# Kernel tuning notes

Measured on AMD Instinct MI355X. Metric: run time of the kernel, lower is better.

## Reference

```python
import jax, jax.numpy as jnp
import numpy as np

D_MODEL = 1024
NUM_HEADS = 16
HEAD_DIM = D_MODEL // NUM_HEADS
WINDOW = 64
GLOBAL_TOKENS = 4
MAX_SEQ_LEN = 2048
RANDOM_TOKENS = 32
BATCH = 2
SEQ = 2048
NEG = -1.0e9
LN_EPS = 1e-5


def setup_inputs() -> dict:
    key = jax.random.key(0)
    k1, k2, k3, k4 = jax.random.split(key, 4)
    x = jax.random.normal(k1, (BATCH, SEQ, D_MODEL), dtype=jnp.float32)
    w_qkv = jax.random.normal(k2, (D_MODEL, 3 * D_MODEL), dtype=jnp.float32) * (D_MODEL ** -0.5)
    w_out = jax.random.normal(k3, (D_MODEL, D_MODEL), dtype=jnp.float32) * (D_MODEL ** -0.5)
    ln_gamma = jnp.ones((D_MODEL,), dtype=jnp.float32)
    ln_beta = jnp.zeros((D_MODEL,), dtype=jnp.float32)
    rand_idx = jax.random.randint(k4, (MAX_SEQ_LEN, RANDOM_TOKENS), 0, MAX_SEQ_LEN, dtype=jnp.int32)
    return {"x": x, "w_qkv": w_qkv, "w_out": w_out,
            "ln_gamma": ln_gamma, "ln_beta": ln_beta, "rand_idx": rand_idx}


def _build_masks(seq_len, rand_idx):
    i = jnp.arange(seq_len)
    causal = (i[:, None] >= i[None, :]).astype(jnp.float32)  # [L,L], lower-triangular
    # local window mask
    dist = jnp.abs(i[:, None] - i[None, :])
    local = (dist <= WINDOW).astype(jnp.float32) * causal
    # global column mask: columns {0..G-1} u {L-G..L-1}, rows i >= g (== causal on those cols)
    gcols = jnp.concatenate([jnp.arange(GLOBAL_TOKENS), jnp.arange(seq_len - GLOBAL_TOKENS, seq_len)])
    is_gcol = jnp.zeros((seq_len,), jnp.float32).at[gcols].set(1.0)
    glob = is_gcol[None, :] * causal
    # random mask: per-row fixed random columns, then causal-filtered
    ri = rand_idx[:seq_len]  # [L, R]
    rows = jnp.broadcast_to(i[:, None], ri.shape)
    rnd = jnp.zeros((seq_len, seq_len), jnp.float32).at[rows, ri].set(1.0) * causal
    return local, glob, rnd


def reference(x, w_qkv, w_out, ln_gamma, ln_beta, rand_idx):
    B, L, _ = x.shape
    residual = x
    # LayerNorm
    mu = jnp.mean(x, axis=-1, keepdims=True)
    var = jnp.mean(jnp.square(x - mu), axis=-1, keepdims=True)
    xn = (x - mu) * jax.lax.rsqrt(var + LN_EPS) * ln_gamma + ln_beta
    # QKV projection
    qkv = xn @ w_qkv
    q, k, v = jnp.split(qkv, 3, axis=-1)
    q = q.reshape(B, L, NUM_HEADS, HEAD_DIM).transpose(0, 2, 1, 3)  # [B,H,L,D]
    k = k.reshape(B, L, NUM_HEADS, HEAD_DIM).transpose(0, 2, 1, 3)
    v = v.reshape(B, L, NUM_HEADS, HEAD_DIM).transpose(0, 2, 1, 3)
    local, glob, rnd = _build_masks(L, rand_idx)
    raw = jnp.einsum('bhqd,bhkd->bhqk', q, k) / jnp.sqrt(jnp.float32(HEAD_DIM))
    # original sums three masked copies of the same scores:
    # combined = 3*raw + ((1-local)+(1-glob)+(1-rnd)) * NEG
    penalty = (3.0 - (local + glob + rnd)) * NEG  # [L,L]
    combined = 3.0 * raw + penalty[None, None, :, :]
    attn = jax.nn.softmax(combined, axis=-1)
    out = jnp.einsum('bhqk,bhkd->bhqd', attn, v)
    out = out.transpose(0, 2, 1, 3).reshape(B, L, D_MODEL)
    out = out @ w_out
    return out + residual
```

## Files before the change

### kernel.cpp

```cpp
#include <hip/hip_runtime.h>
#include <stdint.h>

typedef __attribute__((ext_vector_type(8))) short shortx8;
typedef __attribute__((ext_vector_type(4))) float floatx4;

static constexpr int SEQ_    = 2048;
static constexpr int DMODEL  = 1024;
static constexpr int HDIM    = 64;
static constexpr int BATCH_  = 2;
static constexpr int NHEADS  = 16;
static constexpr int WINDOW_ = 64;
static constexpr int GTOK    = 4;
static constexpr int RTOK    = 32;
static constexpr int ROWS    = BATCH_ * SEQ_;
static constexpr int QKVN    = 3 * DMODEL;

__device__ inline unsigned short f2bf(float f) {
  union { float f; unsigned int u; } x; x.f = f;
  unsigned int r = (x.u + 0x7FFFu + ((x.u >> 16) & 1u)) >> 16;
  return (unsigned short)r;
}
__device__ inline float bf2f(unsigned short b) {
  union { unsigned int u; float f; } x; x.u = ((unsigned int)b) << 16;
  return x.f;
}

__device__ inline void gload_lds16(const void* g, void* l) {
  __builtin_amdgcn_global_load_lds(
      (const __attribute__((address_space(1))) void*)g,
      (__attribute__((address_space(3))) void*)l, 16, 0, 0);
}

__device__ __forceinline__ void gemm_bk64_128x64(
    const unsigned short* __restrict__ aP0, const unsigned short* __restrict__ aP1,
    const unsigned short* __restrict__ aP2, const unsigned short* __restrict__ aP3,
    const unsigned short* __restrict__ bP0, const unsigned short* __restrict__ bP1,
    unsigned short* smem, const int wave, const int lane, floatx4 (&acc)[4][2]) {
  const int quad = lane >> 4, l16 = lane & 15;
  const int wm = (wave >> 1) * 64, wn = (wave & 1) * 32;
  const int h = l16 & 7;
  auto STAGE = [&](int c, int k0) {
    unsigned short* Ad = smem + c * 12288 + wave * 2048;
    unsigned short* Bd = smem + c * 12288 + 8192 + wave * 1024;
    gload_lds16(aP0 + k0, Ad);
    gload_lds16(aP1 + k0, Ad + 512);
    gload_lds16(aP2 + k0, Ad + 1024);
    gload_lds16(aP3 + k0, Ad + 1536);
    gload_lds16(bP0 + k0, Bd);
    gload_lds16(bP1 + k0, Bd + 512);
  };
  auto COMPUTE = [&](int c) {
    const unsigned short* A = smem + c * 12288;
    const unsigned short* B = A + 8192;
    #pragma unroll
    for (int kk = 0; kk < 2; kk++) {
      shortx8 af[4], bfr[2];
      #pragma unroll
      for (int s = 0; s < 4; s++)
        af[s] = *(const shortx8*)&A[(wm + s * 16 + l16) * 64 + (((quad + kk * 4) ^ h) * 8)];
      #pragma unroll
      for (int s = 0; s < 2; s++)
        bfr[s] = *(const shortx8*)&B[(wn + s * 16 + l16) * 64 + (((quad + kk * 4) ^ h) * 8)];
      #pragma unroll
      for (int sm = 0; sm < 4; sm++)
        #pragma unroll
        for (int sn = 0; sn < 2; sn++)
          acc[sm][sn] = __builtin_amdgcn_mfma_f32_16x16x32_bf16(af[sm], bfr[sn], acc[sm][sn], 0, 0, 0);
    }
  };
  STAGE(0, 0);
  int cur = 0;
  #pragma unroll 1
  for (int t = 0; t < 15; ++t) {
    STAGE(cur ^ 1, (t + 1) * 64);
    asm volatile("s_waitcnt vmcnt(6)" ::: "memory");
    __builtin_amdgcn_s_barrier();
    __builtin_amdgcn_sched_barrier(0);
    COMPUTE(cur);
    __builtin_amdgcn_sched_barrier(0);
    __builtin_amdgcn_s_barrier();
    cur ^= 1;
  }
  asm volatile("s_waitcnt vmcnt(0)" ::: "memory");
  __builtin_amdgcn_s_barrier();
  __builtin_amdgcn_sched_barrier(0);
  COMPUTE(cur);
}

__global__ __launch_bounds__(256) void k1_prep(
    const float* __restrict__ x, const float* __restrict__ w_qkv,
    const float* __restrict__ w_out, const float* __restrict__ gamma,
    const float* __restrict__ beta, const int* __restrict__ ridx,
    unsigned short* __restrict__ xn, unsigned short* __restrict__ wqT,
    unsigned short* __restrict__ woT, unsigned short* __restrict__ Wvs,
    int* __restrict__ cols, int* __restrict__ cnt, int* __restrict__ tmx,
    int* __restrict__ cnts2, int* __restrict__ qlist) {
  __shared__ float tile[32][33];
  __shared__ float red[4], red2[4];
  __shared__ int rl[RTOK];
  __shared__ int scw, scnw, stm;
  const int bx = blockIdx.x;
  const int t = threadIdx.x;
  if (bx < 3072) {
    int n0 = (bx % 96) * 32, k0 = (bx / 96) * 32;
    int tx = t & 31, ty = t >> 5;
    #pragma unroll
    for (int r = ty; r < 32; r += 8)
      tile[r][tx] = w_qkv[(size_t)(k0 + r) * QKVN + n0 + tx];
    __syncthreads();
    #pragma unroll
    for (int r = ty; r < 32; r += 8)
      wqT[(size_t)(n0 + r) * DMODEL + k0 + tx] = f2bf(tile[tx][r]);
  } else if (bx < 7168) {
    int row = bx - 3072;
    const float4* xr = (const float4*)(x + (size_t)row * DMODEL);
    float4 v = xr[t];
    float s = v.x + v.y + v.z + v.w;
    #pragma unroll
    for (int o = 32; o > 0; o >>= 1) s += __shfl_xor(s, o);
    int wave = t >> 6, lane = t & 63;
    if (lane == 0) red[wave] = s;
    __syncthreads();
    float mean = (red[0] + red[1] + red[2] + red[3]) * (1.0f / DMODEL);
    float dx = v.x - mean, dy = v.y - mean, dz = v.z - mean, dw = v.w - mean;
    float q = dx*dx + dy*dy + dz*dz + dw*dw;
    #pragma unroll
    for (int o = 32; o > 0; o >>= 1) q += __shfl_xor(q, o);
    if (lane == 0) red2[wave] = q;
    __syncthreads();
    float var = (red2[0] + red2[1] + red2[2] + red2[3]) * (1.0f / DMODEL);
    float rs = rsqrtf(var + 1e-5f);
    float4 g = ((const float4*)gamma)[t];
    float4 bb = ((const float4*)beta)[t];
    ushort4 outv;
    outv.x = f2bf(dx * rs * g.x + bb.x);
    outv.y = f2bf(dy * rs * g.y + bb.y);
    outv.z = f2bf(dz * rs * g.z + bb.z);
    outv.w = f2bf(dw * rs * g.w + bb.w);
    ((ushort4*)(xn + (size_t)row * DMODEL))[t] = outv;
  } else if (bx < 8192) {
    int idx = bx - 7168;
    int n0 = (idx & 31) * 32, k0 = (idx >> 5) * 32;
    int tx = t & 31, ty = t >> 5;
    #pragma unroll
    for (int r = ty; r < 32; r += 8)
      tile[r][tx] = w_out[(size_t)(k0 + r) * DMODEL + n0 + tx];
    __syncthreads();
    #pragma unroll
    for (int r = ty; r < 32; r += 8)
      woT[(size_t)(n0 + r) * DMODEL + k0 + tx] = f2bf(tile[tx][r]);
  } else if (bx < 9216) {
    int idx = bx - 8192;
    int v0 = (idx & 31) * 32, k0 = (idx >> 5) * 32;
    int tx = t & 31, ty = t >> 5;
    #pragma unroll
    for (int r = ty; r < 32; r += 8)
      Wvs[(size_t)(k0 + r) * DMODEL + v0 + tx] =
          f2bf(w_qkv[(size_t)(k0 + r) * QKVN + 2 * DMODEL + v0 + tx]);
  } else {
    const int i = bx - 9216;
    if (t < RTOK) rl[t] = ridx[i * RTOK + t];
    if (t == 0) { scw = 0; scnw = 0; stm = 0; }
    __syncthreads();
    const int wstart = (i - WINDOW_ > 0) ? (i - WINDOW_) : 0;
    const int c = t;
    int j = -1;
    bool valid = false;
    bool iswin = (c < 65);
    if (c < 65) {
      j = i - WINDOW_ + c;
      valid = (j >= 0);
    } else if (c < 73) {
      int g = c - 65;
      j = (g < 4) ? g : (SEQ_ - 8 + g);
      valid = (j <= i) && (j < wstart);
    } else if (c < 73 + RTOK) {
      int r = c - 73;
      j = rl[r];
      bool dup = false;
      for (int r2 = 0; r2 < r; r2++) dup = dup || (rl[r2] == j);
      valid = (j <= i) && (j < wstart) && !(j < GTOK || j >= SEQ_ - GTOK) && !dup;
    }
    int tier = -1;
    if (valid) {
      int loc = ((i - j) <= WINDOW_) ? 1 : 0;
      int glb = (j < GTOK || j >= SEQ_ - GTOK) ? 1 : 0;
      int rnd = 0;
      for (int r = 0; r < RTOK; r++) rnd |= (rl[r] == j) ? 1 : 0;
      tier = loc + glb + rnd;
      atomicMax(&stm, tier);
    }
    __syncthreads();
    const int tm = stm;
    if (valid && tier == tm) {
      if (iswin) {
        int pos = atomicAdd(&scw, 1);
        cols[i * 128 + pos] = j;
      } else {
        int pos = 127 - atomicAdd(&scnw, 1);
        cols[i * 128 + pos] = j;
      }
    }
    __syncthreads();
    if (t == 0) {
      cnt[i] = scw + scnw;
      tmx[i] = tm;
      cnts2[i] = scw | (scnw << 16);
      if (i < 68 || i >= SEQ_ - 4) {
        int cc = (i < 68) ? i : 68 + (i - (SEQ_ - 4));
        qlist[cc * 2 + 0] = (tm == 3) ? i : -1;
        qlist[cc * 2 + 1] = (tm == 3) ? (SEQ_ + i) : -1;
      }
    }
  }
}

__global__ __launch_bounds__(256) void k2_wgemm(
    const unsigned short* __restrict__ woT, const unsigned short* __restrict__ Wvs,
    unsigned short* __restrict__ WvoT, const unsigned short* __restrict__ xn,
    const unsigned short* __restrict__ wqT, const int* __restrict__ qlist,
    unsigned short* __restrict__ qf, unsigned short* __restrict__ kf,
    unsigned short* __restrict__ vf) {
  __shared__ __align__(16) unsigned short smem[2 * 12288];
  const int bx = blockIdx.x, t = threadIdx.x;
  const int wave = t >> 6, lane = t & 63;
  const int quad = lane >> 4, l16 = lane & 15;
  const int wm = (wave >> 1) * 64, wn = (wave & 1) * 32;
  const int r8 = lane >> 3;
  const int swo = ((lane & 7) ^ r8) * 8;
  floatx4 acc[4][2] = {};
  if (bx < 128) {
    const int bm = (bx >> 4) * 128, bn = (bx & 15) * 64;
    const unsigned short* a0 = woT + (size_t)(bm + wave * 32 + r8) * DMODEL + swo;
    const unsigned short* b0 = Wvs + (size_t)(bn + wave * 16 + r8) * DMODEL + swo;
    gemm_bk64_128x64(a0, a0 + 8 * DMODEL, a0 + 16 * DMODEL, a0 + 24 * DMODEL,
                     b0, b0 + 8 * DMODEL, smem, wave, lane, acc);
    #pragma unroll
    for (int sm = 0; sm < 4; sm++)
      #pragma unroll
      for (int sn = 0; sn < 2; sn++)
        #pragma unroll
        for (int r = 0; r < 4; r++) {
          int row = bm + wm + sm * 16 + quad * 4 + r;
          int col = bn + wn + sn * 16 + l16;
          WvoT[(size_t)row * DMODEL + col] = f2bf(acc[sm][sn][r]);
        }
  } else {
    const int idx = bx - 128;
    const int job = idx >> 4, bn = (idx & 15) * 64;
    const int wsel = (job < 2) ? 0 : ((job == 2) ? 1 : 2);
    const unsigned short* BT = wqT + (size_t)wsel * DMODEL * DMODEL;
    unsigned short* dstbuf = (job == 0) ? qf
                           : (job == 1) ? (qf + (size_t)128 * DMODEL)
                           : (job == 2) ? kf : vf;
    const unsigned short* aPg[4];
    #pragma unroll
    for (int g = 0; g < 4; g++) {
      int m = wave * 32 + g * 8 + r8;
      int row;
      if (job < 2) {
        int s = job * 128 + m;
        int ql = (s < 144) ? qlist[s] : -1;
        row = (ql < 0) ? 0 : ql;
      } else {
        row = (m < 16) ? ((m >> 3) * SEQ_ + (((m & 7) < 4) ? (m & 7) : (SEQ_ - 8 + (m & 7)))) : 0;
      }
      aPg[g] = xn + (size_t)row * DMODEL + swo;
    }
    const unsigned short* b0 = BT + (size_t)(bn + wave * 16 + r8) * DMODEL + swo;
    gemm_bk64_128x64(aPg[0], aPg[1], aPg[2], aPg[3],
                     b0, b0 + 8 * DMODEL, smem, wave, lane, acc);
    #pragma unroll
    for (int sm = 0; sm < 4; sm++)
      #pragma unroll
      for (int sn = 0; sn < 2; sn++)
        #pragma unroll
        for (int r = 0; r < 4; r++) {
          int m = wm + sm * 16 + quad * 4 + r;
          int col = bn + wn + sn * 16 + l16;
          dstbuf[(size_t)m * DMODEL + col] = f2bf(acc[sm][sn][r]);
        }
  }
}

__global__ __launch_bounds__(256) void k3_xbar(
    const unsigned short* __restrict__ xn, const int* __restrict__ cols,
    const int* __restrict__ cnt, const int* __restrict__ tmx,
    const int* __restrict__ cnts2, const int* __restrict__ qlist,
    const unsigned short* __restrict__ qf, const unsigned short* __restrict__ kf,
    const unsigned short* __restrict__ vf,
    unsigned short* __restrict__ xbar, unsigned short* __restrict__ vbar) {
  const int bx = blockIdx.x, t = threadIdx.x;
  const int wave = t >> 6, lane = t & 63;
  if (bx < 1024) {
    __shared__ unsigned short win[80][256];
    const int b = bx >> 9, rest = bx & 511;
    const int i0 = (rest >> 2) * 16, dimbase = (rest & 3) * 256;
    const size_t xnb = (size_t)(b * SEQ_) * DMODEL;
    const int lo = i0 - 64;
    const int r0 = i0 + wave * 4;
    int tm_[4], cw_[4], cnw_[4], jr0_[4], jr1_[4];
    #pragma unroll
    for (int rr = 0; rr < 4; rr++) {
      const int i = r0 + rr;
      tm_[rr] = tmx[i];
      int c2 = cnts2[i];
      cw_[rr] = c2 & 0xffff; cnw_[rr] = c2 >> 16;
      jr0_[rr] = cols[i * 128 + lane];
      jr1_[rr] = cols[i * 128 + 64 + lane];
    }
    {
      const int l5 = lane & 31, rsub = lane >> 5;
      #pragma unroll 5
      for (int it = 0; it < 10; it++) {
        int r = it * 8 + wave * 2 + rsub;
        int gr = lo + r;
        if (gr >= 0)
          *(int4*)&win[r][l5 * 8] =
              *(const int4*)(xn + xnb + (size_t)gr * DMODEL + dimbase + l5 * 8);
      }
    }
    __syncthreads();
    const unsigned short* xnd = xn + xnb + dimbase + lane * 4;
    auto add4 = [](float4& s, ushort4 v) {
      s.x += bf2f(v.x); s.y += bf2f(v.y); s.z += bf2f(v.z); s.w += bf2f(v.w);
    };
    auto sub4 = [](float4& s, ushort4 v) {
      s.x -= bf2f(v.x); s.y -= bf2f(v.y); s.z -= bf2f(v.z); s.w -= bf2f(v.w);
    };
    float4 ws = {0, 0, 0, 0};
    {
      float4 t1 = {0,0,0,0}, t2 = {0,0,0,0}, t3 = {0,0,0,0};
      const int jstart = (r0 - 64 > 0) ? (r0 - 64) : 0;
      const int cn = r0 - jstart + 1;
      const int base = jstart - lo;
      int c = 0;
      for (; c + 4 <= cn; c += 4) {
        ushort4 v0 = *(const ushort4*)&win[base + c][lane * 4];
        ushort4 v1 = *(const ushort4*)&win[base + c + 1][lane * 4];
        ushort4 v2 = *(const ushort4*)&win[base + c + 2][lane * 4];
        ushort4 v3 = *(const ushort4*)&win[base + c + 3][lane * 4];
        add4(ws, v0); add4(t1, v1); add4(t2, v2); add4(t3, v3);
      }
      for (; c < cn; c++) add4(ws, *(const ushort4*)&win[base + c][lane * 4]);
      ws.x += t1.x + t2.x + t3.x; ws.y += t1.y + t2.y + t3.y;
      ws.z += t1.z + t2.z + t3.z; ws.w += t1.w + t2.w + t3.w;
    }
    for (int rr = 0; rr < 4; rr++) {
      const int i = r0 + rr;
      if (rr > 0) {
        add4(ws, *(const ushort4*)&win[i - lo][lane * 4]);
        int dj = i - 65;
        if (dj >= 0) sub4(ws, *(const ushort4*)&win[dj - lo][lane * 4]);
      }
      const int tm = tm_[rr];
      ushort4 o;
      if (tm == 3) {
        o.x = o.y = o.z = o.w = 0;
      } else {
        const int cw = cw_[rr], cnw = cnw_[rr];
        const int jr1 = jr1_[rr];
        float4 s;
        if (tm == 1) {
          s = ws;
          float4 t1 = {0,0,0,0}, t2 = {0,0,0,0}, t3 = {0,0,0,0};
          const int bb = 64 - cnw;
          int c = 0;
          for (; c + 8 <= cnw; c += 8) {
            ushort4 v0 = *(const ushort4*)(xnd + (size_t)__shfl(jr1, bb + c)     * DMODEL);
            ushort4 v1 = *(const ushort4*)(xnd + (size_t)__shfl(jr1, bb + c + 1) * DMODEL);
            ushort4 v2 = *(const ushort4*)(xnd + (size_t)__shfl(jr1, bb + c + 2) * DMODEL);
            ushort4 v3 = *(const ushort4*)(xnd + (size_t)__shfl(jr1, bb + c + 3) * DMODEL);
            ushort4 v4 = *(const ushort4*)(xnd + (size_t)__shfl(jr1, bb + c + 4) * DMODEL);
            ushort4 v5 = *(const ushort4*)(xnd + (size_t)__shfl(jr1, bb + c + 5) * DMODEL);
            ushort4 v6 = *(const ushort4*)(xnd + (size_t)__shfl(jr1, bb + c + 6) * DMODEL);
            ushort4 v7 = *(const ushort4*)(xnd + (size_t)__shfl(jr1, bb + c + 7) * DMODEL);
            add4(s, v0); add4(t1, v1); add4(t2, v2); add4(t3, v3);
            add4(s, v4); add4(t1, v5); add4(t2, v6); add4(t3, v7);
          }
          if (c + 4 <= cnw) {
            ushort4 v0 = *(const ushort4*)(xnd + (size_t)__shfl(jr1, bb + c)     * DMODEL);
            ushort4 v1 = *(const ushort4*)(xnd + (size_t)__shfl(jr1, bb + c + 1) * DMODEL);
            ushort4 v2 = *(const ushort4*)(xnd + (size_t)__shfl(jr1, bb + c + 2) * DMODEL);
            ushort4 v3 = *(const ushort4*)(xnd + (size_t)__shfl(jr1, bb + c + 3) * DMODEL);
            add4(s, v0); add4(t1, v1); add4(t2, v2); add4(t3, v3);
            c += 4;
          }
          for (; c < cnw; c++)
            add4(s, *(const ushort4*)(xnd + (size_t)__shfl(jr1, bb + c) * DMODEL));
          s.x += t1.x + t2.x + t3.x; s.y += t1.y + t2.y + t3.y;
          s.z += t1.z + t2.z + t3.z; s.w += t1.w + t2.w + t3.w;
        } else {
          const int jr0 = jr0_[rr];
          s.x = s.y = s.z = s.w = 0.f;
          for (int c = 0; c < cw; c++) {
            int j = (c < 64) ? __shfl(jr0, c) : __shfl(jr1, c - 64);
            add4(s, *(const ushort4*)(xnd + (size_t)j * DMODEL));
          }
          const int bb = 64 - cnw;
          for (int c = 0; c < cnw; c++)
            add4(s, *(const ushort4*)(xnd + (size_t)__shfl(jr1, bb + c) * DMODEL));
        }
        const float inv = 1.0f / (float)(cw + cnw);
        o.x = f2bf(s.x * inv); o.y = f2bf(s.y * inv);
        o.z = f2bf(s.z * inv); o.w = f2bf(s.w * inv);
      }
      *(ushort4*)(xbar + (size_t)(b * SEQ_ + i) * DMODEL + dimbase + lane * 4) = o;
    }
  } else {
    const int s = (bx - 1024) * 4 + wave;
    const int dst = (s < 144) ? qlist[s] : -1;
    if (dst < 0) return;
    const int b = dst >> 11, i = dst & (SEQ_ - 1);
    const int n = cnt[i];
    int myk = 0;
    if (lane < n) {
      int kj = cols[i * 128 + lane];
      myk = b * 8 + ((kj < 4) ? kj : (kj - (SEQ_ - 8)));
    }
    for (int h = 0; h < NHEADS; h++) {
      float qd = bf2f(qf[(size_t)s * DMODEL + h * HDIM + lane]);
      float w[8];
      float m = -1e30f;
      for (int c = 0; c < n; c++) {
        int ks = __shfl(myk, c);
        float kd = bf2f(kf[(size_t)ks * DMODEL + h * HDIM + lane]);
        float p = qd * kd;
        #pragma unroll
        for (int o = 32; o > 0; o >>= 1) p += __shfl_xor(p, o);
        p *= 0.375f;
        w[c] = p;
        m = fmaxf(m, p);
      }
      float denom = 0.f, acc = 0.f;
      for (int c = 0; c < n; c++) {
        int ks = __shfl(myk, c);
        float e = __expf(w[c] - m);
        denom += e;
        acc += e * bf2f(vf[(size_t)ks * DMODEL + h * HDIM + lane]);
      }
      vbar[(size_t)s * DMODEL + h * HDIM + lane] = f2bf(acc / denom);
    }
  }
}

__global__ __launch_bounds__(256) void k4_final(
    const unsigned short* __restrict__ xbar, const unsigned short* __restrict__ WvoT,
    const unsigned short* __restrict__ vbar, const unsigned short* __restrict__ woT,
    const int* __restrict__ qlist, const int* __restrict__ tmx,
    const float* __restrict__ x, float* __restrict__ out) {
  __shared__ __align__(16) unsigned short smem[2 * 12288];
  __shared__ int rowinf[128];
  const int bx = blockIdx.x, t = threadIdx.x;
  const int wave = t >> 6, lane = t & 63;
  const int quad = lane >> 4, l16 = lane & 15;
  const int wm = (wave >> 1) * 64, wn = (wave & 1) * 32;
  const int r8 = lane >> 3;
  const int swo = ((lane & 7) ^ r8) * 8;
  floatx4 acc[4][2] = {};
  if (bx < 512) {
    const int bs = (bx & 7) * 64 + (bx >> 3);
    const int bm = (bs >> 4) * 128, bn = (bs & 15) * 64;
    if (t < 128) rowinf[t] = tmx[(bm + t) & (SEQ_ - 1)];
    const unsigned short* a0 = xbar + (size_t)(bm + wave * 32 + r8) * DMODEL + swo;
    const unsigned short* b0 = WvoT + (size_t)(bn + wave * 16 + r8) * DMODEL + swo;
    gemm_bk64_128x64(a0, a0 + 8 * DMODEL, a0 + 16 * DMODEL, a0 + 24 * DMODEL,
                     b0, b0 + 8 * DMODEL, smem, wave, lane, acc);
    #pragma unroll
    for (int sm = 0; sm < 4; sm++)
      #pragma unroll
      for (int sn = 0; sn < 2; sn++)
        #pragma unroll
        for (int r = 0; r < 4; r++) {
          int m = wm + sm * 16 + quad * 4 + r;
          if (rowinf[m] != 3) {
            int col = bn + wn + sn * 16 + l16;
            size_t off = (size_t)(bm + m) * DMODEL + col;
            out[off] = acc[sm][sn][r] + x[off];
          }
        }
  } else {
    const int idx = bx - 512;
    const int bm = (idx >> 4) * 128, bn = (idx & 15) * 64;
    if (t < 128) {
      int s = bm + t;
      rowinf[t] = (s < 144) ? qlist[s] : -1;
    }
    const unsigned short* a0 = vbar + (size_t)(bm + wave * 32 + r8) * DMODEL + swo;
    const unsigned short* b0 = woT + (size_t)(bn + wave * 16 + r8) * DMODEL + swo;
    gemm_bk64_128x64(a0, a0 + 8 * DMODEL, a0 + 16 * DMODEL, a0 + 24 * DMODEL,
                     b0, b0 + 8 * DMODEL, smem, wave, lane, acc);
    #pragma unroll
    for (int sm = 0; sm < 4; sm++)
      #pragma unroll
      for (int sn = 0; sn < 2; sn++)
        #pragma unroll
        for (int r = 0; r < 4; r++) {
          int m = wm + sm * 16 + quad * 4 + r;
          int dst = rowinf[m];
          if (dst >= 0) {
            int col = bn + wn + sn * 16 + l16;
            size_t off = (size_t)dst * DMODEL + col;
            out[off] = acc[sm][sn][r] + x[off];
          }
        }
  }
}

extern "C" void kernel_launch(void* const* d_in, const int* in_sizes, int n_in,
                              void* d_out, int out_size, void* d_ws, size_t ws_size,
                              hipStream_t stream) {
  const float* x     = (const float*)d_in[0];
  const float* w_qkv = (const float*)d_in[1];
  const float* w_out = (const float*)d_in[2];
  const float* gamma = (const float*)d_in[3];
  const float* beta  = (const float*)d_in[4];
  const int*   ridx  = (const int*)d_in[5];
  float* out = (float*)d_out;

  char* ws = (char*)d_ws;
  size_t off = 0;
  auto alloc = [&](size_t bytes) {
    char* p = ws + off;
    off = (off + bytes + 255) & ~(size_t)255;
    return p;
  };
  unsigned short* xn   = (unsigned short*)alloc((size_t)ROWS * DMODEL * 2);
  unsigned short* wqT  = (unsigned short*)alloc((size_t)QKVN * DMODEL * 2);
  unsigned short* woT  = (unsigned short*)alloc((size_t)DMODEL * DMODEL * 2);
  unsigned short* Wvs  = (unsigned short*)alloc((size_t)DMODEL * DMODEL * 2);
  unsigned short* WvoT = (unsigned short*)alloc((size_t)DMODEL * DMODEL * 2);
  unsigned short* xbar = (unsigned short*)alloc((size_t)ROWS * DMODEL * 2);
  unsigned short* qf   = (unsigned short*)alloc((size_t)256 * DMODEL * 2);
  unsigned short* kf   = (unsigned short*)alloc((size_t)128 * DMODEL * 2);
  unsigned short* vf   = (unsigned short*)alloc((size_t)128 * DMODEL * 2);
  unsigned short* vbar = (unsigned short*)alloc((size_t)256 * DMODEL * 2);
  int* cols  = (int*)alloc((size_t)SEQ_ * 128 * 4);
  int* cnt   = (int*)alloc((size_t)SEQ_ * 4);
  int* tmx   = (int*)alloc((size_t)SEQ_ * 4);
  int* cnts2 = (int*)alloc((size_t)SEQ_ * 4);
  int* qlist = (int*)alloc(256 * 4);

  hipLaunchKernelGGL(k1_prep, dim3(11264), dim3(256), 0, stream,
                     x, w_qkv, w_out, gamma, beta, ridx,
                     xn, wqT, woT, Wvs, cols, cnt, tmx, cnts2, qlist);
  hipLaunchKernelGGL(k2_wgemm, dim3(192), dim3(256), 0, stream,
                     woT, Wvs, WvoT, xn, wqT, qlist, qf, kf, vf);
  hipLaunchKernelGGL(k3_xbar, dim3(1060), dim3(256), 0, stream,
                     xn, cols, cnt, tmx, cnts2, qlist, qf, kf, vf, xbar, vbar);
  hipLaunchKernelGGL(k4_final, dim3(544), dim3(256), 0, stream,
                     xbar, WvoT, vbar, woT, qlist, tmx, x, out);
}
```

Measured before the change: 163.5 us.

## Fuse weight GEMMs with xbar averaging, coarsen prep blocks, split global-row attention

The weight-GEMM blocks and the xbar windowed-averaging blocks now run in one launch, with the windowed part reusing the GEMM's shared memory. The small global-token attention becomes its own kernel launched after that fused kernel. The prep kernel makes each block transpose four 32x32 tiles and gives each LayerNorm row to a single wave using shuffles, which removes the LDS reductions and syncthreads. The in-window accumulation now reads from the LDS window instead of global memory and uses two accumulators to get more ILP. The fused launch mixes heavy GEMM blocks with light averaging blocks, which can unbalance the grid, and the extra small launch adds overhead.

Result: slower. 171.6 us (+4.9%).

```diff
diff --git a/kernel.cpp b/kernel.cpp
--- a/kernel.cpp
+++ b/kernel.cpp
@@ -96,69 +96,89 @@
     int* __restrict__ cols, int* __restrict__ cnt, int* __restrict__ tmx,
     int* __restrict__ cnts2, int* __restrict__ qlist) {
   __shared__ float tile[32][33];
-  __shared__ float red[4], red2[4];
   __shared__ int rl[RTOK];
   __shared__ int scw, scnw, stm;
   const int bx = blockIdx.x;
   const int t = threadIdx.x;
-  if (bx < 3072) {
-    int n0 = (bx % 96) * 32, k0 = (bx / 96) * 32;
-    int tx = t & 31, ty = t >> 5;
-    #pragma unroll
-    for (int r = ty; r < 32; r += 8)
-      tile[r][tx] = w_qkv[(size_t)(k0 + r) * QKVN + n0 + tx];
-    __syncthreads();
-    #pragma unroll
-    for (int r = ty; r < 32; r += 8)
-      wqT[(size_t)(n0 + r) * DMODEL + k0 + tx] = f2bf(tile[tx][r]);
-  } else if (bx < 7168) {
-    int row = bx - 3072;
+  if (bx < 768) {
+    const int n0 = (bx % 24) * 128, k0 = (bx / 24) * 32;
+    const int tx = t & 31, ty = t >> 5;
+    #pragma unroll 1
+    for (int s = 0; s < 4; s++) {
+      const int nb = n0 + s * 32;
+      #pragma unroll
+      for (int r = ty; r < 32; r += 8)
+        tile[r][tx] = w_qkv[(size_t)(k0 + r) * QKVN + nb + tx];
+      __syncthreads();
+      #pragma unroll
+      for (int r = ty; r < 32; r += 8)
+        wqT[(size_t)(nb + r) * DMODEL + k0 + tx] = f2bf(tile[tx][r]);
+      __syncthreads();
+    }
+  } else if (bx < 1792) {
+    const int wave = t >> 6, lane = t & 63;
+    const int row = (bx - 768) * 4 + wave;
     const float4* xr = (const float4*)(x + (size_t)row * DMODEL);
-    float4 v = xr[t];
-    float s = v.x + v.y + v.z + v.w;
+    float4 v[4];
+    #pragma unroll
+    for (int j = 0; j < 4; j++) v[j] = xr[lane + j * 64];
+    float s = 0.f;
+    #pragma unroll
+    for (int j = 0; j < 4; j++) s += v[j].x + v[j].y + v[j].z + v[j].w;
     #pragma unroll
     for (int o = 32; o > 0; o >>= 1) s += __shfl_xor(s, o);
-    int wave = t >> 6, lane = t & 63;
-    if (lane == 0) red[wave] = s;
-    __syncthreads();
-    float mean = (red[0] + red[1] + red[2] + red[3]) * (1.0f / DMODEL);
-    float dx = v.x - mean, dy = v.y - mean, dz = v.z - mean, dw = v.w - mean;
-    float q = dx*dx + dy*dy + dz*dz + dw*dw;
+    const float mean = s * (1.0f / DMODEL);
+    float q = 0.f;
+    #pragma unroll
+    for (int j = 0; j < 4; j++) {
+      float a = v[j].x - mean, b = v[j].y - mean, c = v[j].z - mean, d = v[j].w - mean;
+      q += a * a + b * b + c * c + d * d;
+    }
     #pragma unroll
     for (int o = 32; o > 0; o >>= 1) q += __shfl_xor(q, o);
-    if (lane == 0) red2[wave] = q;
-    __syncthreads();
-    float var = (red2[0] + red2[1] + red2[2] + red2[3]) * (1.0f / DMODEL);
-    float rs = rsqrtf(var + 1e-5f);
-    float4 g = ((const float4*)gamma)[t];
-    float4 bb = ((const float4*)beta)[t];
-    ushort4 outv;
-    outv.x = f2bf(dx * rs * g.x + bb.x);
-    outv.y = f2bf(dy * rs * g.y + bb.y);
-    outv.z = f2bf(dz * rs * g.z + bb.z);
-    outv.w = f2bf(dw * rs * g.w + bb.w);
-    ((ushort4*)(xn + (size_t)row * DMODEL))[t] = outv;
-  } else if (bx < 8192) {
-    int idx = bx - 7168;
-    int n0 = (idx & 31) * 32, k0 = (idx >> 5) * 32;
-    int tx = t & 31, ty = t >> 5;
-    #pragma unroll
-    for (int r = ty; r < 32; r += 8)
-      tile[r][tx] = w_out[(size_t)(k0 + r) * DMODEL + n0 + tx];
-    __syncthreads();
-    #pragma unroll
-    for (int r = ty; r < 32; r += 8)
-      woT[(size_t)(n0 + r) * DMODEL + k0 + tx] = f2bf(tile[tx][r]);
-  } else if (bx < 9216) {
-    int idx = bx - 8192;
-    int v0 = (idx & 31) * 32, k0 = (idx >> 5) * 32;
-    int tx = t & 31, ty = t >> 5;
-    #pragma unroll
-    for (int r = ty; r < 32; r += 8)
-      Wvs[(size_t)(k0 + r) * DMODEL + v0 + tx] =
-          f2bf(w_qkv[(size_t)(k0 + r) * QKVN + 2 * DMODEL + v0 + tx]);
+    const float rs = rsqrtf(q * (1.0f / DMODEL) + 1e-5f);
+    ushort4* xo = (ushort4*)(xn + (size_t)row * DMODEL);
+    #pragma unroll
+    for (int j = 0; j < 4; j++) {
+      float4 g = ((const float4*)gamma)[lane + j * 64];
+      float4 bb = ((const float4*)beta)[lane + j * 64];
+      ushort4 ov;
+      ov.x = f2bf((v[j].x - mean) * rs * g.x + bb.x);
+      ov.y = f2bf((v[j].y - mean) * rs * g.y + bb.y);
+      ov.z = f2bf((v[j].z - mean) * rs * g.z + bb.z);
+      ov.w = f2bf((v[j].w - mean) * rs * g.w + bb.w);
+      xo[lane + j * 64] = ov;
+    }
+  } else if (bx < 2048) {
+    const int idx = bx - 1792;
+    const int n0 = (idx & 7) * 128, k0 = (idx >> 3) * 32;
+    const int tx = t & 31, ty = t >> 5;
+    #pragma unroll 1
+    for (int s = 0; s < 4; s++) {
+      const int nb = n0 + s * 32;
+      #pragma unroll
+      for (int r = ty; r < 32; r += 8)
+        tile[r][tx] = w_out[(size_t)(k0 + r) * DMODEL + nb + tx];
+      __syncthreads();
+      #pragma unroll
+      for (int r = ty; r < 32; r += 8)
+        woT[(size_t)(nb + r) * DMODEL + k0 + tx] = f2bf(tile[tx][r]);
+      __syncthreads();
+    }
+  } else if (bx < 2304) {
+    const int idx = bx - 2048;
+    const int v0 = (idx & 7) * 128, k0 = (idx >> 3) * 32;
+    const int tx = t & 31, ty = t >> 5;
+    #pragma unroll
+    for (int s = 0; s < 4; s++) {
+      const int col = v0 + s * 32 + tx;
+      #pragma unroll
+      for (int r = ty; r < 32; r += 8)
+        Wvs[(size_t)(k0 + r) * DMODEL + col] =
+            f2bf(w_qkv[(size_t)(k0 + r) * QKVN + 2 * DMODEL + col]);
+    }
   } else {
-    const int i = bx - 9216;
+    const int i = bx - 2304;
     if (t < RTOK) rl[t] = ridx[i * RTOK + t];
     if (t == 0) { scw = 0; scnw = 0; stm = 0; }
     __syncthreads();
@@ -215,86 +235,79 @@
   }
 }
 
-__global__ __launch_bounds__(256) void k2_wgemm(
+__global__ __launch_bounds__(256) void k23_fused(
+    const unsigned short* __restrict__ xn, const int* __restrict__ cols,
+    const int* __restrict__ tmx, const int* __restrict__ cnts2,
     const unsigned short* __restrict__ woT, const unsigned short* __restrict__ Wvs,
-    unsigned short* __restrict__ WvoT, const unsigned short* __restrict__ xn,
     const unsigned short* __restrict__ wqT, const int* __restrict__ qlist,
-    unsigned short* __restrict__ qf, unsigned short* __restrict__ kf,
-    unsigned short* __restrict__ vf) {
+    unsigned short* __restrict__ WvoT, unsigned short* __restrict__ qf,
+    unsigned short* __restrict__ kf, unsigned short* __restrict__ vf,
+    unsigned short* __restrict__ xbar) {
   __shared__ __align__(16) unsigned short smem[2 * 12288];
   const int bx = blockIdx.x, t = threadIdx.x;
   const int wave = t >> 6, lane = t & 63;
-  const int quad = lane >> 4, l16 = lane & 15;
-  const int wm = (wave >> 1) * 64, wn = (wave & 1) * 32;
-  const int r8 = lane >> 3;
-  const int swo = ((lane & 7) ^ r8) * 8;
-  floatx4 acc[4][2] = {};
-  if (bx < 128) {
-    const int bm = (bx >> 4) * 128, bn = (bx & 15) * 64;
-    const unsigned short* a0 = woT + (size_t)(bm + wave * 32 + r8) * DMODEL + swo;
-    const unsigned short* b0 = Wvs + (size_t)(bn + wave * 16 + r8) * DMODEL + swo;
-    gemm_bk64_128x64(a0, a0 + 8 * DMODEL, a0 + 16 * DMODEL, a0 + 24 * DMODEL,
-                     b0, b0 + 8 * DMODEL, smem, wave, lane, acc);
-    #pragma unroll
-    for (int sm = 0; sm < 4; sm++)
-      #pragma unroll
-      for (int sn = 0; sn < 2; sn++)
+  if (bx < 192) {
+    const int quad = lane >> 4, l16 = lane & 15;
+    const int wm = (wave >> 1) * 64, wn = (wave & 1) * 32;
+    const int r8 = lane >> 3;
+    const int swo = ((lane & 7) ^ r8) * 8;
+    floatx4 acc[4][2] = {};
+    if (bx < 128) {
+      const int bm = (bx >> 4) * 128, bn = (bx & 15) * 64;
+      const unsigned short* a0 = woT + (size_t)(bm + wave * 32 + r8) * DMODEL + swo;
+      const unsigned short* b0 = Wvs + (size_t)(bn + wave * 16 + r8) * DMODEL + swo;
+      gemm_bk64_128x64(a0, a0 + 8 * DMODEL, a0 + 16 * DMODEL, a0 + 24 * DMODEL,
+                       b0, b0 + 8 * DMODEL, smem, wave, lane, acc);
+      #pragma unroll
+      for (int sm = 0; sm < 4; sm++)
         #pragma unroll
-        for (int r = 0; r < 4; r++) {
-          int row = bm + wm + sm * 16 + quad * 4 + r;
-          int col = bn + wn + sn * 16 + l16;
-          WvoT[(size_t)row * DMODEL + col] = f2bf(acc[sm][sn][r]);
+        for (int sn = 0; sn < 2; sn++)
+          #pragma unroll
+          for (int r = 0; r < 4; r++) {
+            int row = bm + wm + sm * 16 + quad * 4 + r;
+            int col = bn + wn + sn * 16 + l16;
+            WvoT[(size_t)row * DMODEL + col] = f2bf(acc[sm][sn][r]);
+          }
+    } else {
+      const int idx = bx - 128;
+      const int job = idx >> 4, bn = (idx & 15) * 64;
+      const int wsel = (job < 2) ? 0 : ((job == 2) ? 1 : 2);
+      const unsigned short* BT = wqT + (size_t)wsel * DMODEL * DMODEL;
+      unsigned short* dstbuf = (job == 0) ? qf
+                             : (job == 1) ? (qf + (size_t)128 * DMODEL)
+                             : (job == 2) ? kf : vf;
+      const unsigned short* aPg[4];
+      #pragma unroll
+      for (int g = 0; g < 4; g++) {
+        int m = wave * 32 + g * 8 + r8;
+        int row;
+        if (job < 2) {
+          int s = job * 128 + m;
+          int ql = (s < 144) ? qlist[s] : -1;
+          row = (ql < 0) ? 0 : ql;
+        } else {
+          row = (m < 16) ? ((m >> 3) * SEQ_ + (((m & 7) < 4) ? (m & 7) : (SEQ_ - 8 + (m & 7)))) : 0;
         }
+        aPg[g] = xn + (size_t)row * DMODEL + swo;
+      }
+      const unsigned short* b0 = BT + (size_t)(bn + wave * 16 + r8) * DMODEL + swo;
+      gemm_bk64_128x64(aPg[0], aPg[1], aPg[2], aPg[3],
+                       b0, b0 + 8 * DMODEL, smem, wave, lane, acc);
+      #pragma unroll
+      for (int sm = 0; sm < 4; sm++)
+        #pragma unroll
+        for (int sn = 0; sn < 2; sn++)
+          #pragma unroll
+          for (int r = 0; r < 4; r++) {
+            int m = wm + sm * 16 + quad * 4 + r;
+            int col = bn + wn + sn * 16 + l16;
+            dstbuf[(size_t)m * DMODEL + col] = f2bf(acc[sm][sn][r]);
+          }
+    }
   } else {
-    const int idx = bx - 128;
-    const int job = idx >> 4, bn = (idx & 15) * 64;
-    const int wsel = (job < 2) ? 0 : ((job == 2) ? 1 : 2);
-    const unsigned short* BT = wqT + (size_t)wsel * DMODEL * DMODEL;
-    unsigned short* dstbuf = (job == 0) ? qf
-                           : (job == 1) ? (qf + (size_t)128 * DMODEL)
-                           : (job == 2) ? kf : vf;
-    const unsigned short* aPg[4];
-    #pragma unroll
-    for (int g = 0; g < 4; g++) {
-      int m = wave * 32 + g * 8 + r8;
-      int row;
-      if (job < 2) {
-        int s = job * 128 + m;
-        int ql = (s < 144) ? qlist[s] : -1;
-        row = (ql < 0) ? 0 : ql;
-      } else {
-        row = (m < 16) ? ((m >> 3) * SEQ_ + (((m & 7) < 4) ? (m & 7) : (SEQ_ - 8 + (m & 7)))) : 0;
-      }
-      aPg[g] = xn + (size_t)row * DMODEL + swo;
-    }
-    const unsigned short* b0 = BT + (size_t)(bn + wave * 16 + r8) * DMODEL + swo;
-    gemm_bk64_128x64(aPg[0], aPg[1], aPg[2], aPg[3],
-                     b0, b0 + 8 * DMODEL, smem, wave, lane, acc);
-    #pragma unroll
-    for (int sm = 0; sm < 4; sm++)
-      #pragma unroll
-      for (int sn = 0; sn < 2; sn++)
-        #pragma unroll
-        for (int r = 0; r < 4; r++) {
-          int m = wm + sm * 16 + quad * 4 + r;
-          int col = bn + wn + sn * 16 + l16;
-          dstbuf[(size_t)m * DMODEL + col] = f2bf(acc[sm][sn][r]);
-        }
-  }
-}
-
-__global__ __launch_bounds__(256) void k3_xbar(
-    const unsigned short* __restrict__ xn, const int* __restrict__ cols,
-    const int* __restrict__ cnt, const int* __restrict__ tmx,
-    const int* __restrict__ cnts2, const int* __restrict__ qlist,
-    const unsigned short* __restrict__ qf, const unsigned short* __restrict__ kf,
-    const unsigned short* __restrict__ vf,
-    unsigned short* __restrict__ xbar, unsigned short* __restrict__ vbar) {
-  const int bx = blockIdx.x, t = threadIdx.x;
-  const int wave = t >> 6, lane = t & 63;
-  if (bx < 1024) {
-    __shared__ unsigned short win[80][256];
-    const int b = bx >> 9, rest = bx & 511;
+    auto win = reinterpret_cast<unsigned short (*)[256]>(smem);
+    const int xb = bx - 192;
+    const int b = xb >> 9, rest = xb & 511;
     const int i0 = (rest >> 2) * 16, dimbase = (rest & 3) * 256;
     const size_t xnb = (size_t)(b * SEQ_) * DMODEL;
     const int lo = i0 - 64;
@@ -393,13 +406,28 @@
         } else {
           const int jr0 = jr0_[rr];
           s.x = s.y = s.z = s.w = 0.f;
-          for (int c = 0; c < cw; c++) {
+          float4 t1 = {0,0,0,0};
+          int c = 0;
+          for (; c + 2 <= cw; c += 2) {
+            int j0 = (c < 64)     ? __shfl(jr0, c)     : __shfl(jr1, c - 64);
+            int j1 = (c + 1 < 64) ? __shfl(jr0, c + 1) : __shfl(jr1, c - 63);
+            add4(s,  *(const ushort4*)&win[j0 - lo][lane * 4]);
+            add4(t1, *(const ushort4*)&win[j1 - lo][lane * 4]);
+          }
+          if (c < cw) {
             int j = (c < 64) ? __shfl(jr0, c) : __shfl(jr1, c - 64);
-            add4(s, *(const ushort4*)(xnd + (size_t)j * DMODEL));
+            add4(s, *(const ushort4*)&win[j - lo][lane * 4]);
           }
           const int bb = 64 - cnw;
-          for (int c = 0; c < cnw; c++)
+          c = 0;
+          for (; c + 2 <= cnw; c += 2) {
+            ushort4 v0 = *(const ushort4*)(xnd + (size_t)__shfl(jr1, bb + c)     * DMODEL);
+            ushort4 v1 = *(const ushort4*)(xnd + (size_t)__shfl(jr1, bb + c + 1) * DMODEL);
+            add4(s, v0); add4(t1, v1);
+          }
+          if (c < cnw)
             add4(s, *(const ushort4*)(xnd + (size_t)__shfl(jr1, bb + c) * DMODEL));
+          s.x += t1.x; s.y += t1.y; s.z += t1.z; s.w += t1.w;
         }
         const float inv = 1.0f / (float)(cw + cnw);
         o.x = f2bf(s.x * inv); o.y = f2bf(s.y * inv);
@@ -407,40 +435,48 @@
       }
       *(ushort4*)(xbar + (size_t)(b * SEQ_ + i) * DMODEL + dimbase + lane * 4) = o;
     }
-  } else {
-    const int s = (bx - 1024) * 4 + wave;
-    const int dst = (s < 144) ? qlist[s] : -1;
-    if (dst < 0) return;
-    const int b = dst >> 11, i = dst & (SEQ_ - 1);
-    const int n = cnt[i];
-    int myk = 0;
-    if (lane < n) {
-      int kj = cols[i * 128 + lane];
-      myk = b * 8 + ((kj < 4) ? kj : (kj - (SEQ_ - 8)));
-    }
-    for (int h = 0; h < NHEADS; h++) {
-      float qd = bf2f(qf[(size_t)s * DMODEL + h * HDIM + lane]);
-      float w[8];
-      float m = -1e30f;
-      for (int c = 0; c < n; c++) {
-        int ks = __shfl(myk, c);
-        float kd = bf2f(kf[(size_t)ks * DMODEL + h * HDIM + lane]);
-        float p = qd * kd;
-        #pragma unroll
-        for (int o = 32; o > 0; o >>= 1) p += __shfl_xor(p, o);
-        p *= 0.375f;
-        w[c] = p;
-        m = fmaxf(m, p);
-      }
-      float denom = 0.f, acc = 0.f;
-      for (int c = 0; c < n; c++) {
-        int ks = __shfl(myk, c);
-        float e = __expf(w[c] - m);
-        denom += e;
-        acc += e * bf2f(vf[(size_t)ks * DMODEL + h * HDIM + lane]);
-      }
-      vbar[(size_t)s * DMODEL + h * HDIM + lane] = f2bf(acc / denom);
-    }
+  }
+}
+
+__global__ __launch_bounds__(256) void k3_t3(
+    const int* __restrict__ cols, const int* __restrict__ cnt,
+    const int* __restrict__ qlist,
+    const unsigned short* __restrict__ qf, const unsigned short* __restrict__ kf,
+    const unsigned short* __restrict__ vf, unsigned short* __restrict__ vbar) {
+  const int t = threadIdx.x;
+  const int wave = t >> 6, lane = t & 63;
+  const int s = blockIdx.x * 4 + wave;
+  const int dst = (s < 144) ? qlist[s] : -1;
+  if (dst < 0) return;
+  const int b = dst >> 11, i = dst & (SEQ_ - 1);
+  const int n = cnt[i];
+  int myk = 0;
+  if (lane < n) {
+    int kj = cols[i * 128 + lane];
+    myk = b * 8 + ((kj < 4) ? kj : (kj - (SEQ_ - 8)));
+  }
+  for (int h = 0; h < NHEADS; h++) {
+    float qd = bf2f(qf[(size_t)s * DMODEL + h * HDIM + lane]);
+    float w[8];
+    float m = -1e30f;
+    for (int c = 0; c < n; c++) {
+      int ks = __shfl(myk, c);
+      float kd = bf2f(kf[(size_t)ks * DMODEL + h * HDIM + lane]);
+      float p = qd * kd;
+      #pragma unroll
+      for (int o = 32; o > 0; o >>= 1) p += __shfl_xor(p, o);
+      p *= 0.375f;
+      w[c] = p;
+      m = fmaxf(m, p);
+    }
+    float denom = 0.f, acc = 0.f;
+    for (int c = 0; c < n; c++) {
+      int ks = __shfl(myk, c);
+      float e = __expf(w[c] - m);
+      denom += e;
+      acc += e * bf2f(vf[(size_t)ks * DMODEL + h * HDIM + lane]);
+    }
+    vbar[(size_t)s * DMODEL + h * HDIM + lane] = f2bf(acc / denom);
   }
 }
 
@@ -541,13 +577,14 @@
   int* cnts2 = (int*)alloc((size_t)SEQ_ * 4);
   int* qlist = (int*)alloc(256 * 4);
 
-  hipLaunchKernelGGL(k1_prep, dim3(11264), dim3(256), 0, stream,
+  hipLaunchKernelGGL(k1_prep, dim3(4352), dim3(256), 0, stream,
                      x, w_qkv, w_out, gamma, beta, ridx,
                      xn, wqT, woT, Wvs, cols, cnt, tmx, cnts2, qlist);
-  hipLaunchKernelGGL(k2_wgemm, dim3(192), dim3(256), 0, stream,
-                     woT, Wvs, WvoT, xn, wqT, qlist, qf, kf, vf);
-  hipLaunchKernelGGL(k3_xbar, dim3(1060), dim3(256), 0, stream,
-                     xn, cols, cnt, tmx, cnts2, qlist, qf, kf, vf, xbar, vbar);
+  hipLaunchKernelGGL(k23_fused, dim3(1216), dim3(256), 0, stream,
+                     xn, cols, tmx, cnts2, woT, Wvs, wqT, qlist,
+                     WvoT, qf, kf, vf, xbar);
+  hipLaunchKernelGGL(k3_t3, dim3(36), dim3(256), 0, stream,
+                     cols, cnt, qlist, qf, kf, vf, vbar);
   hipLaunchKernelGGL(k4_final, dim3(544), dim3(256), 0, stream,
                      xbar, WvoT, vbar, woT, qlist, tmx, x, out);
 }
```

## Fuse weight GEMMs with xbar gather into one launch, split tiny attention kernel

Applied to the files above, without the earlier changes.

The weight-product and q/k/v projection GEMM blocks now share one launch with the xbar gather blocks, so the small 192-block GEMM no longer runs alone with the GPU mostly idle. The global-token attention part is split into its own small kernel because it depends on the GEMM outputs. A new BK=32 GEMM helper uses less shared memory so the fused kernel fits the gather's LDS window. The gather's window-column loop now reads from LDS instead of global memory and uses two accumulators. Risks are lower GEMM efficiency with the smaller K tile and an extra launch.

Result: slower. 171.5 us (+4.9%).

```diff
diff --git a/kernel.cpp b/kernel.cpp
--- a/kernel.cpp
+++ b/kernel.cpp
@@ -87,6 +87,55 @@
   COMPUTE(cur);
 }
 
+__device__ __forceinline__ void gemm_bk32_128x64(
+    const unsigned short* __restrict__ aP0, const unsigned short* __restrict__ aP1,
+    const unsigned short* __restrict__ bP0,
+    unsigned short* smem, const int wave, const int lane, floatx4 (&acc)[4][2]) {
+  const int quad = lane >> 4, l16 = lane & 15;
+  const int wm = (wave >> 1) * 64, wn = (wave & 1) * 32;
+  const int ch = (quad ^ (l16 & 3)) * 8;
+  auto STAGE = [&](int c, int k0) {
+    unsigned short* Ad = smem + c * 6144 + wave * 1024;
+    unsigned short* Bd = smem + c * 6144 + 4096 + wave * 512;
+    gload_lds16(aP0 + k0, Ad);
+    gload_lds16(aP1 + k0, Ad + 512);
+    gload_lds16(bP0 + k0, Bd);
+  };
+  auto COMPUTE = [&](int c) {
+    const unsigned short* A = smem + c * 6144;
+    const unsigned short* B = A + 4096;
+    shortx8 af[4], bfr[2];
+    #pragma unroll
+    for (int s = 0; s < 4; s++)
+      af[s] = *(const shortx8*)&A[(wm + s * 16 + l16) * 32 + ch];
+    #pragma unroll
+    for (int s = 0; s < 2; s++)
+      bfr[s] = *(const shortx8*)&B[(wn + s * 16 + l16) * 32 + ch];
+    #pragma unroll
+    for (int sm = 0; sm < 4; sm++)
+      #pragma unroll
+      for (int sn = 0; sn < 2; sn++)
+        acc[sm][sn] = __builtin_amdgcn_mfma_f32_16x16x32_bf16(af[sm], bfr[sn], acc[sm][sn], 0, 0, 0);
+  };
+  STAGE(0, 0);
+  int cur = 0;
+  #pragma unroll 1
+  for (int t = 0; t < 31; ++t) {
+    STAGE(cur ^ 1, (t + 1) * 32);
+    asm volatile("s_waitcnt vmcnt(3)" ::: "memory");
+    __builtin_amdgcn_s_barrier();
+    __builtin_amdgcn_sched_barrier(0);
+    COMPUTE(cur);
+    __builtin_amdgcn_sched_barrier(0);
+    __builtin_amdgcn_s_barrier();
+    cur ^= 1;
+  }
+  asm volatile("s_waitcnt vmcnt(0)" ::: "memory");
+  __builtin_amdgcn_s_barrier();
+  __builtin_amdgcn_sched_barrier(0);
+  COMPUTE(cur);
+}
+
 __global__ __launch_bounds__(256) void k1_prep(
     const float* __restrict__ x, const float* __restrict__ w_qkv,
     const float* __restrict__ w_out, const float* __restrict__ gamma,
@@ -215,86 +264,77 @@
   }
 }
 
-__global__ __launch_bounds__(256) void k2_wgemm(
+__global__ __launch_bounds__(256) void k23_fused(
+    const unsigned short* __restrict__ xn, const int* __restrict__ cols,
+    const int* __restrict__ tmx, const int* __restrict__ cnts2,
     const unsigned short* __restrict__ woT, const unsigned short* __restrict__ Wvs,
-    unsigned short* __restrict__ WvoT, const unsigned short* __restrict__ xn,
     const unsigned short* __restrict__ wqT, const int* __restrict__ qlist,
-    unsigned short* __restrict__ qf, unsigned short* __restrict__ kf,
-    unsigned short* __restrict__ vf) {
-  __shared__ __align__(16) unsigned short smem[2 * 12288];
+    unsigned short* __restrict__ WvoT, unsigned short* __restrict__ qf,
+    unsigned short* __restrict__ kf, unsigned short* __restrict__ vf,
+    unsigned short* __restrict__ xbar) {
+  __shared__ __align__(16) unsigned short smem[80 * 256];
   const int bx = blockIdx.x, t = threadIdx.x;
   const int wave = t >> 6, lane = t & 63;
-  const int quad = lane >> 4, l16 = lane & 15;
-  const int wm = (wave >> 1) * 64, wn = (wave & 1) * 32;
-  const int r8 = lane >> 3;
-  const int swo = ((lane & 7) ^ r8) * 8;
-  floatx4 acc[4][2] = {};
-  if (bx < 128) {
-    const int bm = (bx >> 4) * 128, bn = (bx & 15) * 64;
-    const unsigned short* a0 = woT + (size_t)(bm + wave * 32 + r8) * DMODEL + swo;
-    const unsigned short* b0 = Wvs + (size_t)(bn + wave * 16 + r8) * DMODEL + swo;
-    gemm_bk64_128x64(a0, a0 + 8 * DMODEL, a0 + 16 * DMODEL, a0 + 24 * DMODEL,
-                     b0, b0 + 8 * DMODEL, smem, wave, lane, acc);
-    #pragma unroll
-    for (int sm = 0; sm < 4; sm++)
-      #pragma unroll
-      for (int sn = 0; sn < 2; sn++)
+  if (bx < 192) {
+    const int quad = lane >> 4, l16 = lane & 15;
+    const int wm = (wave >> 1) * 64, wn = (wave & 1) * 32;
+    const int rr4 = lane >> 2;
+    const int swo = (((lane & 3) ^ (rr4 & 3)) * 8);
+    floatx4 acc[4][2] = {};
+    if (bx < 128) {
+      const int bm = (bx >> 4) * 128, bn = (bx & 15) * 64;
+      const unsigned short* a0 = woT + (size_t)(bm + wave * 32 + rr4) * DMODEL + swo;
+      const unsigned short* b0 = Wvs + (size_t)(bn + wave * 16 + rr4) * DMODEL + swo;
+      gemm_bk32_128x64(a0, a0 + 16 * DMODEL, b0, smem, wave, lane, acc);
+      #pragma unroll
+      for (int sm = 0; sm < 4; sm++)
         #pragma unroll
-        for (int r = 0; r < 4; r++) {
-          int row = bm + wm + sm * 16 + quad * 4 + r;
-          int col = bn + wn + sn * 16 + l16;
-          WvoT[(size_t)row * DMODEL + col] = f2bf(acc[sm][sn][r]);
+        for (int sn = 0; sn < 2; sn++)
+          #pragma unroll
+          for (int r = 0; r < 4; r++) {
+            int row = bm + wm + sm * 16 + quad * 4 + r;
+            int col = bn + wn + sn * 16 + l16;
+            WvoT[(size_t)row * DMODEL + col] = f2bf(acc[sm][sn][r]);
+          }
+    } else {
+      const int idx = bx - 128;
+      const int job = idx >> 4, bn = (idx & 15) * 64;
+      const int wsel = (job < 2) ? 0 : ((job == 2) ? 1 : 2);
+      const unsigned short* BT = wqT + (size_t)wsel * DMODEL * DMODEL;
+      unsigned short* dstbuf = (job == 0) ? qf
+                             : (job == 1) ? (qf + (size_t)128 * DMODEL)
+                             : (job == 2) ? kf : vf;
+      const unsigned short* aPg[2];
+      #pragma unroll
+      for (int g = 0; g < 2; g++) {
+        int m = wave * 32 + g * 16 + rr4;
+        int row;
+        if (job < 2) {
+          int s = job * 128 + m;
+          int ql = (s < 144) ? qlist[s] : -1;
+          row = (ql < 0) ? 0 : ql;
+        } else {
+          row = (m < 16) ? ((m >> 3) * SEQ_ + (((m & 7) < 4) ? (m & 7) : (SEQ_ - 8 + (m & 7)))) : 0;
         }
+        aPg[g] = xn + (size_t)row * DMODEL + swo;
+      }
+      const unsigned short* b0 = BT + (size_t)(bn + wave * 16 + rr4) * DMODEL + swo;
+      gemm_bk32_128x64(aPg[0], aPg[1], b0, smem, wave, lane, acc);
+      #pragma unroll
+      for (int sm = 0; sm < 4; sm++)
+        #pragma unroll
+        for (int sn = 0; sn < 2; sn++)
+          #pragma unroll
+          for (int r = 0; r < 4; r++) {
+            int m = wm + sm * 16 + quad * 4 + r;
+            int col = bn + wn + sn * 16 + l16;
+            dstbuf[(size_t)m * DMODEL + col] = f2bf(acc[sm][sn][r]);
+          }
+    }
   } else {
-    const int idx = bx - 128;
-    const int job = idx >> 4, bn = (idx & 15) * 64;
-    const int wsel = (job < 2) ? 0 : ((job == 2) ? 1 : 2);
-    const unsigned short* BT = wqT + (size_t)wsel * DMODEL * DMODEL;
-    unsigned short* dstbuf = (job == 0) ? qf
-                           : (job == 1) ? (qf + (size_t)128 * DMODEL)
-                           : (job == 2) ? kf : vf;
-    const unsigned short* aPg[4];
-    #pragma unroll
-    for (int g = 0; g < 4; g++) {
-      int m = wave * 32 + g * 8 + r8;
-      int row;
-      if (job < 2) {
-        int s = job * 128 + m;
-        int ql = (s < 144) ? qlist[s] : -1;
-        row = (ql < 0) ? 0 : ql;
-      } else {
-        row = (m < 16) ? ((m >> 3) * SEQ_ + (((m & 7) < 4) ? (m & 7) : (SEQ_ - 8 + (m & 7)))) : 0;
-      }
-      aPg[g] = xn + (size_t)row * DMODEL + swo;
-    }
-    const unsigned short* b0 = BT + (size_t)(bn + wave * 16 + r8) * DMODEL + swo;
-    gemm_bk64_128x64(aPg[0], aPg[1], aPg[2], aPg[3],
-                     b0, b0 + 8 * DMODEL, smem, wave, lane, acc);
-    #pragma unroll
-    for (int sm = 0; sm < 4; sm++)
-      #pragma unroll
-      for (int sn = 0; sn < 2; sn++)
-        #pragma unroll
-        for (int r = 0; r < 4; r++) {
-          int m = wm + sm * 16 + quad * 4 + r;
-          int col = bn + wn + sn * 16 + l16;
-          dstbuf[(size_t)m * DMODEL + col] = f2bf(acc[sm][sn][r]);
-        }
-  }
-}
-
-__global__ __launch_bounds__(256) void k3_xbar(
-    const unsigned short* __restrict__ xn, const int* __restrict__ cols,
-    const int* __restrict__ cnt, const int* __restrict__ tmx,
-    const int* __restrict__ cnts2, const int* __restrict__ qlist,
-    const unsigned short* __restrict__ qf, const unsigned short* __restrict__ kf,
-    const unsigned short* __restrict__ vf,
-    unsigned short* __restrict__ xbar, unsigned short* __restrict__ vbar) {
-  const int bx = blockIdx.x, t = threadIdx.x;
-  const int wave = t >> 6, lane = t & 63;
-  if (bx < 1024) {
-    __shared__ unsigned short win[80][256];
-    const int b = bx >> 9, rest = bx & 511;
+    auto win = reinterpret_cast<unsigned short (*)[256]>(smem);
+    const int xb = bx - 192;
+    const int b = xb >> 9, rest = xb & 511;
     const int i0 = (rest >> 2) * 16, dimbase = (rest & 3) * 256;
     const size_t xnb = (size_t)(b * SEQ_) * DMODEL;
     const int lo = i0 - 64;
@@ -393,13 +433,28 @@
         } else {
           const int jr0 = jr0_[rr];
           s.x = s.y = s.z = s.w = 0.f;
-          for (int c = 0; c < cw; c++) {
+          float4 t1 = {0,0,0,0};
+          int c = 0;
+          for (; c + 2 <= cw; c += 2) {
+            int j0 = (c < 64)     ? __shfl(jr0, c)     : __shfl(jr1, c - 64);
+            int j1 = (c + 1 < 64) ? __shfl(jr0, c + 1) : __shfl(jr1, c - 63);
+            add4(s,  *(const ushort4*)&win[j0 - lo][lane * 4]);
+            add4(t1, *(const ushort4*)&win[j1 - lo][lane * 4]);
+          }
+          if (c < cw) {
             int j = (c < 64) ? __shfl(jr0, c) : __shfl(jr1, c - 64);
-            add4(s, *(const ushort4*)(xnd + (size_t)j * DMODEL));
+            add4(s, *(const ushort4*)&win[j - lo][lane * 4]);
           }
           const int bb = 64 - cnw;
-          for (int c = 0; c < cnw; c++)
+          c = 0;
+          for (; c + 2 <= cnw; c += 2) {
+            ushort4 v0 = *(const ushort4*)(xnd + (size_t)__shfl(jr1, bb + c)     * DMODEL);
+            ushort4 v1 = *(const ushort4*)(xnd + (size_t)__shfl(jr1, bb + c + 1) * DMODEL);
+            add4(s, v0); add4(t1, v1);
+          }
+          if (c < cnw)
             add4(s, *(const ushort4*)(xnd + (size_t)__shfl(jr1, bb + c) * DMODEL));
+          s.x += t1.x; s.y += t1.y; s.z += t1.z; s.w += t1.w;
         }
         const float inv = 1.0f / (float)(cw + cnw);
         o.x = f2bf(s.x * inv); o.y = f2bf(s.y * inv);
@@ -407,40 +462,48 @@
       }
       *(ushort4*)(xbar + (size_t)(b * SEQ_ + i) * DMODEL + dimbase + lane * 4) = o;
     }
-  } else {
-    const int s = (bx - 1024) * 4 + wave;
-    const int dst = (s < 144) ? qlist[s] : -1;
-    if (dst < 0) return;
-    const int b = dst >> 11, i = dst & (SEQ_ - 1);
-    const int n = cnt[i];
-    int myk = 0;
-    if (lane < n) {
-      int kj = cols[i * 128 + lane];
-      myk = b * 8 + ((kj < 4) ? kj : (kj - (SEQ_ - 8)));
-    }
-    for (int h = 0; h < NHEADS; h++) {
-      float qd = bf2f(qf[(size_t)s * DMODEL + h * HDIM + lane]);
-      float w[8];
-      float m = -1e30f;
-      for (int c = 0; c < n; c++) {
-        int ks = __shfl(myk, c);
-        float kd = bf2f(kf[(size_t)ks * DMODEL + h * HDIM + lane]);
-        float p = qd * kd;
-        #pragma unroll
-        for (int o = 32; o > 0; o >>= 1) p += __shfl_xor(p, o);
-        p *= 0.375f;
-        w[c] = p;
-        m = fmaxf(m, p);
-      }
-      float denom = 0.f, acc = 0.f;
-      for (int c = 0; c < n; c++) {
-        int ks = __shfl(myk, c);
-        float e = __expf(w[c] - m);
-        denom += e;
-        acc += e * bf2f(vf[(size_t)ks * DMODEL + h * HDIM + lane]);
-      }
-      vbar[(size_t)s * DMODEL + h * HDIM + lane] = f2bf(acc / denom);
-    }
+  }
+}
+
+__global__ __launch_bounds__(256) void k3_t3(
+    const int* __restrict__ cols, const int* __restrict__ cnt,
+    const int* __restrict__ qlist,
+    const unsigned short* __restrict__ qf, const unsigned short* __restrict__ kf,
+    const unsigned short* __restrict__ vf, unsigned short* __restrict__ vbar) {
+  const int t = threadIdx.x;
+  const int wave = t >> 6, lane = t & 63;
+  const int s = blockIdx.x * 4 + wave;
+  const int dst = (s < 144) ? qlist[s] : -1;
+  if (dst < 0) return;
+  const int b = dst >> 11, i = dst & (SEQ_ - 1);
+  const int n = cnt[i];
+  int myk = 0;
+  if (lane < n) {
+    int kj = cols[i * 128 + lane];
+    myk = b * 8 + ((kj < 4) ? kj : (kj - (SEQ_ - 8)));
+  }
+  for (int h = 0; h < NHEADS; h++) {
+    float qd = bf2f(qf[(size_t)s * DMODEL + h * HDIM + lane]);
+    float w[8];
+    float m = -1e30f;
+    for (int c = 0; c < n; c++) {
+      int ks = __shfl(myk, c);
+      float kd = bf2f(kf[(size_t)ks * DMODEL + h * HDIM + lane]);
+      float p = qd * kd;
+      #pragma unroll
+      for (int o = 32; o > 0; o >>= 1) p += __shfl_xor(p, o);
+      p *= 0.375f;
+      w[c] = p;
+      m = fmaxf(m, p);
+    }
+    float denom = 0.f, acc = 0.f;
+    for (int c = 0; c < n; c++) {
+      int ks = __shfl(myk, c);
+      float e = __expf(w[c] - m);
+      denom += e;
+      acc += e * bf2f(vf[(size_t)ks * DMODEL + h * HDIM + lane]);
+    }
+    vbar[(size_t)s * DMODEL + h * HDIM + lane] = f2bf(acc / denom);
   }
 }
 
@@ -544,10 +607,11 @@
   hipLaunchKernelGGL(k1_prep, dim3(11264), dim3(256), 0, stream,
                      x, w_qkv, w_out, gamma, beta, ridx,
                      xn, wqT, woT, Wvs, cols, cnt, tmx, cnts2, qlist);
-  hipLaunchKernelGGL(k2_wgemm, dim3(192), dim3(256), 0, stream,
-                     woT, Wvs, WvoT, xn, wqT, qlist, qf, kf, vf);
-  hipLaunchKernelGGL(k3_xbar, dim3(1060), dim3(256), 0, stream,
-                     xn, cols, cnt, tmx, cnts2, qlist, qf, kf, vf, xbar, vbar);
+  hipLaunchKernelGGL(k23_fused, dim3(1216), dim3(256), 0, stream,
+                     xn, cols, tmx, cnts2, woT, Wvs, wqT, qlist,
+                     WvoT, qf, kf, vf, xbar);
+  hipLaunchKernelGGL(k3_t3, dim3(36), dim3(256), 0, stream,
+                     cols, cnt, qlist, qf, kf, vf, vbar);
   hipLaunchKernelGGL(k4_final, dim3(544), dim3(256), 0, stream,
                      xbar, WvoT, vbar, woT, qlist, tmx, x, out);
 }
```
